# Optimization experiments

Hardware: AMD Instinct MI355X
Metric: run time of the kernel (lower is better)

The kernel has to match this reference:

```python
import jax, jax.numpy as jnp
import numpy as np
from jax.scipy.linalg import solve_triangular

REG = 1e-6  # reg_covar added to covariance diagonal
LOG2PI = float(np.log(2.0 * np.pi))
RESP_EPS = 10.0 * float(np.finfo(np.float32).eps)


def _log_gauss(X, means, covs):
    # X: [N,D], means: [K,D], covs: [K,D,D] -> per-sample per-component log N(x|mu_k, Sigma_k): [N,K]
    K, D = means.shape
    eye = jnp.eye(D, dtype=X.dtype)
    chol = jnp.linalg.cholesky(covs + REG * eye)                      # [K,D,D]
    diff = X[None, :, :] - means[:, None, :]                          # [K,N,D]
    sol = jax.vmap(lambda L, d: solve_triangular(L, d.T, lower=True))(chol, diff)  # [K,D,N]
    maha = jnp.sum(sol * sol, axis=1)                                 # [K,N]
    logdet = jnp.sum(jnp.log(jnp.diagonal(chol, axis1=1, axis2=2)), axis=1)  # [K] = 0.5*log|Sigma|
    return (-0.5 * (D * LOG2PI + maha) - logdet[:, None]).T           # [N,K]


def _em_step(X, weights, means, covs):
    N, D = X.shape
    # E-step: responsibilities via stable logsumexp
    lp = _log_gauss(X, means, covs) + jnp.log(weights)[None, :]       # [N,K]
    log_norm = jax.scipy.special.logsumexp(lp, axis=1)                # [N]
    resp = jnp.exp(lp - log_norm[:, None])                            # [N,K]
    # M-step (MLE)
    nk = resp.sum(axis=0) + RESP_EPS                                  # [K]
    new_w = nk / N
    new_means = (resp.T @ X) / nk[:, None]                            # [K,D]
    diff = X[None, :, :] - new_means[:, None, :]                      # [K,N,D]
    new_covs = jnp.einsum('kn,knd,kne->kde', resp.T, diff, diff) / nk[:, None, None]
    new_covs = new_covs + REG * jnp.eye(D, dtype=X.dtype)
    return new_w, new_means, new_covs


def reference(X, weights, means, covariances, n_iter):
    # Normalize provided weights (uniform init in the torch module)
    w0 = weights / jnp.sum(weights)

    def step(carry, _):
        w, m, c = carry
        return _em_step(X, w, m, c), None

    (w, m, c), _ = jax.lax.scan(step, (w0, means, covariances), xs=None, length=n_iter)
    # Final per-sample log-likelihood under the fitted mixture (lower bound)
    lp = _log_gauss(X, m, c) + jnp.log(w)[None, :]
    return jax.scipy.special.logsumexp(lp, axis=1)                    # [N]


def setup_inputs() -> dict:
    key = jax.random.key(0)
    kx, km = jax.random.split(key)
    N, D, K = 100000, 32, 16
    X = jax.random.normal(kx, (N, D), dtype=jnp.float32)
    weights = jnp.ones((K,), dtype=jnp.float32) / K
    means = jax.random.normal(km, (K, D), dtype=jnp.float32)
    covariances = jnp.tile(jnp.eye(D, dtype=jnp.float32)[None], (K, 1, 1))
    return {"X": X, "weights": weights, "means": means, "covariances": covariances, "n_iter": 5}
```

## Files before the change

kernel.cpp:

```cpp
#include <hip/hip_runtime.h>
#include <math.h>

#define REGC 1e-6f
#define LOG2PI 1.83787706640934534f
#define RESP_EPS 1.1920929e-6f

#define NPART_MAX 256
#define PART_K 1156
#define PART_BLK (16 * PART_K)
#define RS 16

typedef __attribute__((ext_vector_type(8))) short short8;
typedef __attribute__((ext_vector_type(4))) float f32x4;
typedef unsigned short ushort_t;
typedef unsigned int uint_t;

__device__ __forceinline__ ushort_t f2bf(float x) {
    uint_t u = __float_as_uint(x);
    uint_t r = (u + 0x7fffu + ((u >> 16) & 1u)) >> 16;
    return (ushort_t)r;
}
__device__ __forceinline__ float bf2f(ushort_t h) {
    return __uint_as_float(((uint_t)h) << 16);
}
__device__ __forceinline__ f32x4 shx4(f32x4 v, int m) {
    f32x4 r;
#pragma unroll
    for (int i = 0; i < 4; ++i) r[i] = __shfl_xor(v[i], m);
    return r;
}
__device__ __forceinline__ f32x4 sel4(bool s, f32x4 b, f32x4 a) {
    f32x4 r;
#pragma unroll
    for (int i = 0; i < 4; ++i) r[i] = s ? b[i] : a[i];
    return r;
}

__global__ void gmm_init(const float* __restrict__ w, const float* __restrict__ mu,
                         const float* __restrict__ cov, float* __restrict__ P0) {
    int t = blockIdx.x * 256 + threadIdx.x;
    if (t < 16) {
        float s = 0.f;
        for (int i = 0; i < 16; ++i) s += w[i];
        P0[t] = w[t] / s;
    } else if (t < 528) {
        P0[t] = mu[t - 16];
    } else if (t < 16912) {
        P0[t] = cov[t - 528];
    }
}

__global__ __launch_bounds__(256) void gmm_xsplit(const float* __restrict__ X,
                                                  ushort_t* __restrict__ Xh,
                                                  ushort_t* __restrict__ Xl,
                                                  ushort_t* __restrict__ XTH,
                                                  int N) {
    int chunk = blockIdx.x;
    int t = threadIdx.x;
    __shared__ float xsh[32][33];
    int s = t >> 3, q = t & 7;
    int n = chunk * 32 + s;
    float4 v = make_float4(0.f, 0.f, 0.f, 0.f);
    if (n < N) v = ((const float4*)(X + (size_t)n * 32))[q];
    float vv[4] = { v.x, v.y, v.z, v.w };
    xsh[s][q * 4 + 0] = v.x; xsh[s][q * 4 + 1] = v.y;
    xsh[s][q * 4 + 2] = v.z; xsh[s][q * 4 + 3] = v.w;
    if (n < N) {
        ushort_t h[4], l[4];
#pragma unroll
        for (int i = 0; i < 4; ++i) {
            h[i] = f2bf(vv[i]);
            l[i] = f2bf(vv[i] - bf2f(h[i]));
        }
        size_t o = (size_t)n * 32 + q * 4;
        uint2 hp = make_uint2((uint_t)h[0] | ((uint_t)h[1] << 16),
                              (uint_t)h[2] | ((uint_t)h[3] << 16));
        uint2 lp = make_uint2((uint_t)l[0] | ((uint_t)l[1] << 16),
                              (uint_t)l[2] | ((uint_t)l[3] << 16));
        *(uint2*)(Xh + o) = hp;
        *(uint2*)(Xl + o) = lp;
    }
    __syncthreads();
    int di = t >> 7;
    int lane = (t >> 1) & 63;
    int jj0 = (t & 1) * 4;
    int c = lane & 15, quad = lane >> 4;
    int d = di * 16 + c;
    ushort_t fh[4];
#pragma unroll
    for (int i = 0; i < 4; ++i) fh[i] = f2bf(xsh[quad * 8 + jj0 + i][d]);
    size_t fo = ((size_t)(chunk * 2 + di) * 64 + lane) * 8 + jj0;
    uint2 hp = make_uint2((uint_t)fh[0] | ((uint_t)fh[1] << 16),
                          (uint_t)fh[2] | ((uint_t)fh[3] << 16));
    *(uint2*)(XTH + fo) = hp;
}

__global__ __launch_bounds__(64) void gmm_prep(const float* __restrict__ P,
                                               ushort_t* __restrict__ Wh,
                                               ushort_t* __restrict__ Wl,
                                               float* __restrict__ Bv,
                                               float* __restrict__ Cc) {
    int k = blockIdx.x;
    int t = threadIdx.x;
    __shared__ float L[32][33];
    __shared__ float Ai[32][33];
    const float* cov = P + 528 + k * 1024;
    const float* mu  = P + 16 + k * 32;

#pragma unroll
    for (int rep = 0; rep < 16; ++rep) {
        int idx = rep * 64 + t;
        int i = idx >> 5, j = idx & 31;
        L[i][j] = cov[idx] + (i == j ? REGC : 0.f);
    }
    __syncthreads();

#pragma unroll
    for (int j = 0; j < 32; ++j) {
        float s = L[j][j];
#pragma unroll
        for (int p = 0; p < j; ++p) { float v = L[j][p]; s -= v * v; }
        float dj = sqrtf(s);
        if (t > j && t < 32) {
            float s2 = L[t][j];
#pragma unroll
            for (int p = 0; p < j; ++p) s2 -= L[t][p] * L[j][p];
            L[t][j] = s2 / dj;
        }
        if (t == j) L[j][j] = dj;
        __syncthreads();
    }

    if (t < 32) {
        float ai[32];
#pragma unroll
        for (int r = 0; r < 32; ++r) {
            float s = (r == t) ? 1.f : 0.f;
#pragma unroll
            for (int p = 0; p < r; ++p) s -= L[r][p] * ai[p];
            ai[r] = s / L[r][r];
        }
#pragma unroll
        for (int r = 0; r < 32; ++r) Ai[r][t] = ai[r];
    }
    __syncthreads();

#pragma unroll
    for (int rep = 0; rep < 16; ++rep) {
        int idx = rep * 64 + t;
        int i = idx >> 5, j = idx & 31;
        float v = Ai[i][j];
        ushort_t h = f2bf(v);
        Wh[(size_t)(k * 32 + i) * 32 + j] = h;
        Wl[(size_t)(k * 32 + i) * 32 + j] = f2bf(v - bf2f(h));
    }
    if (t < 32) {
        float s = 0.f;
#pragma unroll
        for (int j = 0; j < 32; ++j) s += Ai[t][j] * mu[j];
        Bv[k * 32 + t] = s;
    }
    float lv = (t < 32) ? logf(L[t & 31][t & 31]) : 0.f;
#pragma unroll
    for (int off = 1; off < 32; off <<= 1) lv += __shfl_xor(lv, off);
    if (t == 0) Cc[k] = logf(P[k]) - 0.5f * 32.0f * LOG2PI - lv;
}

__global__ __launch_bounds__(256, 2) void gmm_estep(const ushort_t* __restrict__ Xh,
                                                    const ushort_t* __restrict__ Xl,
                                                    const ushort_t* __restrict__ Wh,
                                                    const ushort_t* __restrict__ Wl,
                                                    const float* __restrict__ Bv,
                                                    const float* __restrict__ Cc,
                                                    float* __restrict__ resp,
                                                    float* __restrict__ out,
                                                    int N, int mode) {
    int t = threadIdx.x;
    int wave = t >> 6, lane = t & 63;
    int quad = lane >> 4, c = lane & 15;
    int wstart = (blockIdx.x * 4 + wave) * 32;
    if (wstart + 32 > N) wstart = (N >= 32) ? (N - 32) : 0;
    bool al4 = ((N & 3) == 0);

    size_t xo0 = (size_t)(wstart + c) * 32 + quad * 8;
    size_t xo1 = (size_t)(wstart + 16 + c) * 32 + quad * 8;
    short8 ah0 = *(const short8*)(Xh + xo0);
    short8 al0 = *(const short8*)(Xl + xo0);
    short8 ah1 = *(const short8*)(Xh + xo1);
    short8 al1 = *(const short8*)(Xl + xo1);

    f32x4 p0[2], p1[2], p2[2], p3[2], fin[2];

#pragma unroll
    for (int k = 0; k < 16; ++k) {
        size_t w0 = (size_t)(k * 32 + c) * 32 + quad * 8;
        size_t w1 = w0 + 512;
        short8 bh0 = *(const short8*)(Wh + w0);
        short8 bl0 = *(const short8*)(Wl + w0);
        short8 bh1 = *(const short8*)(Wh + w1);
        short8 bl1 = *(const short8*)(Wl + w1);
        float bv0 = Bv[k * 32 + c];
        float bv1 = Bv[k * 32 + 16 + c];
#pragma unroll
        for (int tt = 0; tt < 2; ++tt) {
            short8 ah = tt ? ah1 : ah0;
            short8 al = tt ? al1 : al0;
            f32x4 a0 = {0.f, 0.f, 0.f, 0.f};
            f32x4 a1 = {0.f, 0.f, 0.f, 0.f};
            a0 = __builtin_amdgcn_mfma_f32_16x16x32_bf16(ah, bh0, a0, 0, 0, 0);
            a0 = __builtin_amdgcn_mfma_f32_16x16x32_bf16(ah, bl0, a0, 0, 0, 0);
            a0 = __builtin_amdgcn_mfma_f32_16x16x32_bf16(al, bh0, a0, 0, 0, 0);
            a1 = __builtin_amdgcn_mfma_f32_16x16x32_bf16(ah, bh1, a1, 0, 0, 0);
            a1 = __builtin_amdgcn_mfma_f32_16x16x32_bf16(ah, bl1, a1, 0, 0, 0);
            a1 = __builtin_amdgcn_mfma_f32_16x16x32_bf16(al, bh1, a1, 0, 0, 0);
            f32x4 ms;
#pragma unroll
            for (int r = 0; r < 4; ++r) {
                float d0 = a0[r] - bv0;
                float d1 = a1[r] - bv1;
                ms[r] = fmaf(d0, d0, d1 * d1);
            }
            if ((k & 1) == 0) { p0[tt] = ms; }
            else {
                f32x4 a = p0[tt] + shx4(p0[tt], 1);
                f32x4 b = ms + shx4(ms, 1);
                f32x4 v = sel4((c & 1) != 0, b, a);
                if ((k & 2) == 0) { p1[tt] = v; }
                else {
                    a = p1[tt] + shx4(p1[tt], 2); b = v + shx4(v, 2); v = sel4((c & 2) != 0, b, a);
                    if ((k & 4) == 0) { p2[tt] = v; }
                    else {
                        a = p2[tt] + shx4(p2[tt], 4); b = v + shx4(v, 4); v = sel4((c & 4) != 0, b, a);
                        if ((k & 8) == 0) { p3[tt] = v; }
                        else {
                            a = p3[tt] + shx4(p3[tt], 8); b = v + shx4(v, 8);
                            fin[tt] = sel4((c & 8) != 0, b, a);
                        }
                    }
                }
            }
        }
    }

    float cc = Cc[c];
#pragma unroll
    for (int tt = 0; tt < 2; ++tt) {
        f32x4 lp;
#pragma unroll
        for (int r = 0; r < 4; ++r) lp[r] = cc - 0.5f * fin[tt][r];
        f32x4 mx = lp;
#pragma unroll
        for (int off = 1; off < 16; off <<= 1) {
            f32x4 s = shx4(mx, off);
#pragma unroll
            for (int r = 0; r < 4; ++r) mx[r] = fmaxf(mx[r], s[r]);
        }
        f32x4 e;
#pragma unroll
        for (int r = 0; r < 4; ++r) e[r] = __expf(lp[r] - mx[r]);
        f32x4 sm = e;
#pragma unroll
        for (int off = 1; off < 16; off <<= 1) sm = sm + shx4(sm, off);

        int nb = wstart + tt * 16 + quad * 4;
        if (mode) {
            if (c == 0) {
                f32x4 o;
#pragma unroll
                for (int r = 0; r < 4; ++r) o[r] = mx[r] + __logf(sm[r]);
                if (al4) *(f32x4*)(out + nb) = o;
                else { for (int r = 0; r < 4; ++r) out[nb + r] = o[r]; }
            }
        } else {
            f32x4 sv;
#pragma unroll
            for (int r = 0; r < 4; ++r) sv[r] = e[r] / sm[r];
            size_t off = (size_t)c * N + nb;
            if (al4) *(f32x4*)(resp + off) = sv;
            else { for (int r = 0; r < 4; ++r) resp[off + r] = sv[r]; }
        }
    }
}

__global__ __launch_bounds__(1024, 4) void gmm_moment(const ushort_t* __restrict__ XTH,
                                                      const float* __restrict__ resp,
                                                      float* __restrict__ part,
                                                      int N, int NC) {
    int t = threadIdx.x;
    int k = t >> 6;
    int lane = t & 63;
    int quad = lane >> 4, c = lane & 15;
    bool al4 = ((N & 3) == 0);

    f32x4 acc00 = {0.f,0.f,0.f,0.f}, acc01 = {0.f,0.f,0.f,0.f};
    f32x4 acc10 = {0.f,0.f,0.f,0.f}, acc11 = {0.f,0.f,0.f,0.f};
    float row0 = 0.f, row1 = 0.f, corner = 0.f;

#pragma unroll 1
    for (int chunk = blockIdx.x; chunk < NC; chunk += gridDim.x) {
        size_t fb = ((size_t)chunk * 2 * 64 + lane) * 8;
        short8 bh0 = *(const short8*)(XTH + fb);
        short8 bh1 = *(const short8*)(XTH + fb + 512);

        const float* rp = resp + (size_t)k * N + (size_t)chunk * 32 + quad * 8;
        float r[8];
        if (al4) {
            float4 ra = *(const float4*)rp;
            float4 rb = *(const float4*)(rp + 4);
            r[0]=ra.x; r[1]=ra.y; r[2]=ra.z; r[3]=ra.w;
            r[4]=rb.x; r[5]=rb.y; r[6]=rb.z; r[7]=rb.w;
        } else {
#pragma unroll
            for (int j = 0; j < 8; ++j) r[j] = rp[j];
        }
        corner += ((r[0]+r[1])+(r[2]+r[3])) + ((r[4]+r[5])+(r[6]+r[7]));

        short8 a0, a1;
#pragma unroll
        for (int jj = 0; jj < 8; ++jj) {
            float x0 = bf2f((ushort_t)bh0[jj]);
            float av0 = r[jj] * x0;
            a0[jj] = (short)f2bf(av0);
            row0 += av0;
            float x1 = bf2f((ushort_t)bh1[jj]);
            float av1 = r[jj] * x1;
            a1[jj] = (short)f2bf(av1);
            row1 += av1;
        }

        acc00 = __builtin_amdgcn_mfma_f32_16x16x32_bf16(a0, bh0, acc00, 0, 0, 0);
        acc01 = __builtin_amdgcn_mfma_f32_16x16x32_bf16(a0, bh1, acc01, 0, 0, 0);
        acc10 = __builtin_amdgcn_mfma_f32_16x16x32_bf16(a1, bh0, acc10, 0, 0, 0);
        acc11 = __builtin_amdgcn_mfma_f32_16x16x32_bf16(a1, bh1, acc11, 0, 0, 0);
    }

    row0 += __shfl_xor(row0, 16);  row0 += __shfl_xor(row0, 32);
    row1 += __shfl_xor(row1, 16);  row1 += __shfl_xor(row1, 32);
    corner += __shfl_xor(corner, 16);  corner += __shfl_xor(corner, 32);

    float* pb = part + ((size_t)blockIdx.x * 16 + k) * PART_K;
#pragma unroll
    for (int r = 0; r < 4; ++r) {
        pb[(quad * 4 + r) * 34 + c]            = acc00[r];
        pb[(quad * 4 + r) * 34 + 16 + c]       = acc01[r];
        pb[(16 + quad * 4 + r) * 34 + c]       = acc10[r];
        pb[(16 + quad * 4 + r) * 34 + 16 + c]  = acc11[r];
    }
    if (quad == 0) {
        pb[32 * 34 + c]      = row0;
        pb[32 * 34 + 16 + c] = row1;
    }
    if (lane == 0) pb[32 * 34 + 32] = corner;
}

__global__ __launch_bounds__(256) void gmm_reduce1(const float* __restrict__ part,
                                                   float* __restrict__ part2,
                                                   int npart) {
    int k = blockIdx.x, g = blockIdx.y;
    int nb = (npart + RS - 1) / RS;
    int b0 = g * nb;
    int b1 = b0 + nb; if (b1 > npart) b1 = npart;
    for (int idx = threadIdx.x; idx < PART_K; idx += 256) {
        float s = 0.f;
#pragma unroll 4
        for (int b = b0; b < b1; ++b)
            s += part[((size_t)b * 16 + k) * PART_K + idx];
        part2[((size_t)g * 16 + k) * PART_K + idx] = s;
    }
}

__global__ __launch_bounds__(256) void gmm_redfin_prep(const float* __restrict__ part2,
                                                       ushort_t* __restrict__ Wh,
                                                       ushort_t* __restrict__ Wl,
                                                       float* __restrict__ Bv,
                                                       float* __restrict__ Cc,
                                                       int N) {
    int k = blockIdx.x;
    int t = threadIdx.x;
    __shared__ float S[1156];
    __shared__ float L[32][33];
    __shared__ float Ai[32][33];

    for (int idx = t; idx < 1156; idx += 256) {
        float s = 0.f;
#pragma unroll
        for (int b = 0; b < RS; ++b)
            s += part2[((size_t)b * 16 + k) * PART_K + idx];
        S[idx] = s;
    }
    __syncthreads();
    float nk = S[32 * 34 + 32] + RESP_EPS;
    float inv = 1.f / nk;
    for (int idx = t; idx < 1024; idx += 256) {
        int i = idx >> 5, j = idx & 31;
        float mi = S[32 * 34 + i] * inv;
        float mj = S[32 * 34 + j] * inv;
        L[i][j] = S[i * 34 + j] * inv - mi * mj + ((i == j) ? 2.f * REGC : 0.f);
    }
    __syncthreads();

#pragma unroll
    for (int j = 0; j < 32; ++j) {
        if (t < 32) {
            float s = L[j][j];
#pragma unroll
            for (int p = 0; p < j; ++p) { float v = L[j][p]; s -= v * v; }
            float dj = sqrtf(s);
            if (t > j) {
                float s2 = L[t][j];
#pragma unroll
                for (int p = 0; p < j; ++p) s2 -= L[t][p] * L[j][p];
                L[t][j] = s2 / dj;
            }
            if (t == j) L[j][j] = dj;
        }
        __syncthreads();
    }

    if (t < 32) {
        float ai[32];
#pragma unroll
        for (int r = 0; r < 32; ++r) {
            float s = (r == t) ? 1.f : 0.f;
#pragma unroll
            for (int p = 0; p < r; ++p) s -= L[r][p] * ai[p];
            ai[r] = s / L[r][r];
        }
#pragma unroll
        for (int r = 0; r < 32; ++r) Ai[r][t] = ai[r];
    }
    __syncthreads();

#pragma unroll
    for (int rep = 0; rep < 4; ++rep) {
        int idx = rep * 256 + t;
        int i = idx >> 5, j = idx & 31;
        float v = Ai[i][j];
        ushort_t h = f2bf(v);
        Wh[(size_t)(k * 32 + i) * 32 + j] = h;
        Wl[(size_t)(k * 32 + i) * 32 + j] = f2bf(v - bf2f(h));
    }
    if (t < 32) {
        float s = 0.f;
#pragma unroll
        for (int j = 0; j < 32; ++j) s += Ai[t][j] * (S[32 * 34 + j] * inv);
        Bv[k * 32 + t] = s;
    }
    float lv = (t < 32) ? logf(L[t & 31][t & 31]) : 0.f;
#pragma unroll
    for (int off = 1; off < 32; off <<= 1) lv += __shfl_xor(lv, off);
    if (t == 0) Cc[k] = logf(nk / (float)N) - 0.5f * 32.0f * LOG2PI - lv;
}

extern "C" void kernel_launch(void* const* d_in, const int* in_sizes, int n_in,
                              void* d_out, int out_size, void* d_ws, size_t ws_size,
                              hipStream_t stream) {
    const float* X   = (const float*)d_in[0];
    const float* w   = (const float*)d_in[1];
    const float* mu  = (const float*)d_in[2];
    const float* cov = (const float*)d_in[3];
    const int NITER = 5;
    int N = in_sizes[0] / 32;
    int NC = (N + 31) / 32;

    float* ws = (float*)d_ws;
    float*    P0 = ws;
    float*    Bv = ws + 16912;
    float*    Cc = ws + 17424;
    ushort_t* Wh = (ushort_t*)(ws + 17440);
    ushort_t* Wl = (ushort_t*)(ws + 25632);
    ushort_t* Xh = (ushort_t*)(ws + 33824);
    ushort_t* Xl = (ushort_t*)(ws + 33824 + (size_t)16 * N);
    size_t xt0 = 33824 + (size_t)32 * N;
    size_t SZ  = (size_t)NC * 512;
    ushort_t* XTH = (ushort_t*)(ws + xt0);
    float*  resp = ws + xt0 + SZ;
    size_t p2base = xt0 + SZ + (size_t)16 * N;
    float*  part2 = ws + p2base;
    size_t pbase = p2base + (size_t)RS * 16 * PART_K;
    float*  part = ws + pbase;

    long long avail = (long long)(ws_size / 4) - (long long)pbase;
    int npart = (int)(avail / PART_BLK);
    if (npart > NPART_MAX) npart = NPART_MAX;
    if (npart < 1) npart = 1;

    float* out = (float*)d_out;

    int eblocks = ((N + 31) / 32 + 3) / 4;

    gmm_init<<<67, 256, 0, stream>>>(w, mu, cov, P0);
    gmm_xsplit<<<NC, 256, 0, stream>>>(X, Xh, Xl, XTH, N);
    gmm_prep<<<16, 64, 0, stream>>>(P0, Wh, Wl, Bv, Cc);

    for (int it = 0; it < NITER; ++it) {
        gmm_estep<<<eblocks, 256, 0, stream>>>(Xh, Xl, Wh, Wl, Bv, Cc, resp, out, N, 0);
        gmm_moment<<<npart, 1024, 0, stream>>>(XTH, resp, part, N, NC);
        dim3 r1(16, RS);
        gmm_reduce1<<<r1, 256, 0, stream>>>(part, part2, npart);
        gmm_redfin_prep<<<16, 256, 0, stream>>>(part2, Wh, Wl, Bv, Cc, N);
    }
    gmm_estep<<<eblocks, 256, 0, stream>>>(Xh, Xl, Wh, Wl, Bv, Cc, resp, out, N, 1);
}
```

Before: 478.1 us.

## Fuse whole EM loop into one cooperative persistent kernel with grid syncs

Replaces the chain of roughly twenty launches (init, split, prep, then per-iteration estep/moment/reduce/finalize) with a single cooperative kernel. It runs one 1024-thread block per 512 samples and uses grid.sync between phases. Responsibilities stay in shared memory instead of a global resp array, X fragments are loaded once into registers, and the moment partials feed directly into a 16-block Cholesky stage. This removes launch gaps and global resp traffic, but requires every block to be co-resident. The final reduction also reads about 196 partials serially per component in only 16 blocks, and the old multi-kernel path is kept as a fallback if the cooperative launch fails.

```diff
diff --git a/kernel.cpp b/kernel.cpp
--- a/kernel.cpp
+++ b/kernel.cpp
@@ -1,5 +1,8 @@
 #include <hip/hip_runtime.h>
+#include <hip/hip_cooperative_groups.h>
 #include <math.h>
+
+namespace cg = cooperative_groups;
 
 #define REGC 1e-6f
 #define LOG2PI 1.83787706640934534f
@@ -34,6 +37,325 @@
 #pragma unroll
     for (int i = 0; i < 4; ++i) r[i] = s ? b[i] : a[i];
     return r;
+}
+
+__device__ __forceinline__ void chol_emit(float* Ls, float* Aif, const float* mean,
+                                          float logwk, int k,
+                                          ushort_t* Wh, ushort_t* Wl,
+                                          float* Bv, float* Cc) {
+    int t = threadIdx.x;
+#pragma unroll
+    for (int j = 0; j < 32; ++j) {
+        if (t < 32) {
+            float s = Ls[j * 33 + j];
+#pragma unroll
+            for (int p = 0; p < j; ++p) { float v = Ls[j * 33 + p]; s -= v * v; }
+            float dj = sqrtf(s);
+            if (t > j) {
+                float s2 = Ls[t * 33 + j];
+#pragma unroll
+                for (int p = 0; p < j; ++p) s2 -= Ls[t * 33 + p] * Ls[j * 33 + p];
+                Ls[t * 33 + j] = s2 / dj;
+            }
+            if (t == j) Ls[j * 33 + j] = dj;
+        }
+        __syncthreads();
+    }
+    if (t < 32) {
+        float ai[32];
+#pragma unroll
+        for (int r = 0; r < 32; ++r) {
+            float s = (r == t) ? 1.f : 0.f;
+#pragma unroll
+            for (int p = 0; p < r; ++p) s -= Ls[r * 33 + p] * ai[p];
+            ai[r] = s / Ls[r * 33 + r];
+        }
+#pragma unroll
+        for (int r = 0; r < 32; ++r) Aif[r * 33 + t] = ai[r];
+    }
+    __syncthreads();
+    {
+        int i = t >> 5, j = t & 31;
+        float v = Aif[i * 33 + j];
+        ushort_t h = f2bf(v);
+        Wh[(size_t)(k * 32 + i) * 32 + j] = h;
+        Wl[(size_t)(k * 32 + i) * 32 + j] = f2bf(v - bf2f(h));
+    }
+    if (t < 32) {
+        float s = 0.f;
+#pragma unroll
+        for (int j = 0; j < 32; ++j) s += Aif[t * 33 + j] * mean[j];
+        Bv[k * 32 + t] = s;
+    }
+    float lv = (t < 32) ? logf(Ls[t * 33 + t]) : 0.f;
+#pragma unroll
+    for (int off = 1; off < 32; off <<= 1) lv += __shfl_xor(lv, off);
+    if (t == 0) Cc[k] = logwk - 0.5f * 32.0f * LOG2PI - lv;
+}
+
+__global__ __launch_bounds__(1024, 4) void gmm_mega(
+    const float* __restrict__ X, const float* __restrict__ w,
+    const float* __restrict__ mu, const float* __restrict__ cov,
+    ushort_t* __restrict__ Xh, ushort_t* __restrict__ Xl,
+    ushort_t* __restrict__ XTH,
+    ushort_t* __restrict__ Wh, ushort_t* __restrict__ Wl,
+    float* __restrict__ Bv, float* __restrict__ Cc,
+    float* __restrict__ part, float* __restrict__ out,
+    int N, int niter) {
+    cg::grid_group grid = cg::this_grid();
+    __shared__ float smem[16 * 516];
+    float (*rsh)[516] = (float (*)[516])smem;
+
+    int t = threadIdx.x;
+    int wave = t >> 6, lane = t & 63;
+    int quad = lane >> 4, c = lane & 15;
+    int bbase = (int)blockIdx.x * 512;
+    bool al4 = ((N & 3) == 0);
+
+#pragma unroll 1
+    for (int rr = 0; rr < 4; ++rr) {
+        int ch = rr * 4 + (t >> 8);
+        int tl = t & 255;
+        float* xsh = smem + (t >> 8) * 1056;
+        int gc = (int)blockIdx.x * 16 + ch;
+        int s = tl >> 3, q = tl & 7;
+        int n = gc * 32 + s;
+        float4 v = make_float4(0.f, 0.f, 0.f, 0.f);
+        if (n < N) v = ((const float4*)(X + (size_t)n * 32))[q];
+        xsh[s * 33 + q * 4 + 0] = v.x; xsh[s * 33 + q * 4 + 1] = v.y;
+        xsh[s * 33 + q * 4 + 2] = v.z; xsh[s * 33 + q * 4 + 3] = v.w;
+        if (n < N) {
+            float vv[4] = { v.x, v.y, v.z, v.w };
+            ushort_t h[4], l[4];
+#pragma unroll
+            for (int i = 0; i < 4; ++i) {
+                h[i] = f2bf(vv[i]);
+                l[i] = f2bf(vv[i] - bf2f(h[i]));
+            }
+            size_t o = (size_t)n * 32 + q * 4;
+            *(uint2*)(Xh + o) = make_uint2((uint_t)h[0] | ((uint_t)h[1] << 16),
+                                           (uint_t)h[2] | ((uint_t)h[3] << 16));
+            *(uint2*)(Xl + o) = make_uint2((uint_t)l[0] | ((uint_t)l[1] << 16),
+                                           (uint_t)l[2] | ((uint_t)l[3] << 16));
+        }
+        __syncthreads();
+        int di = tl >> 7;
+        int lane2 = (tl >> 1) & 63;
+        int jj0 = (tl & 1) * 4;
+        int c2 = lane2 & 15, quad2 = lane2 >> 4;
+        int d = di * 16 + c2;
+        ushort_t fh[4];
+#pragma unroll
+        for (int i2 = 0; i2 < 4; ++i2) fh[i2] = f2bf(xsh[(quad2 * 8 + jj0 + i2) * 33 + d]);
+        size_t fo = ((size_t)(gc * 2 + di) * 64 + lane2) * 8 + jj0;
+        *(uint2*)(XTH + fo) = make_uint2((uint_t)fh[0] | ((uint_t)fh[1] << 16),
+                                         (uint_t)fh[2] | ((uint_t)fh[3] << 16));
+        __syncthreads();
+    }
+
+    if (blockIdx.x < 16) {
+        int k = (int)blockIdx.x;
+        float* Ls = smem + 1156;
+        float* Aif = smem + 2212;
+        {
+            int i = t >> 5, j = t & 31;
+            Ls[i * 33 + j] = cov[(size_t)k * 1024 + t] + ((i == j) ? REGC : 0.f);
+        }
+        float wsum = 0.f;
+#pragma unroll
+        for (int i = 0; i < 16; ++i) wsum += w[i];
+        float logwk = logf(w[k] / wsum);
+        __syncthreads();
+        chol_emit(Ls, Aif, mu + (size_t)k * 32, logwk, k, Wh, Wl, Bv, Cc);
+    }
+    grid.sync();
+    __threadfence();
+
+    int wstart0 = bbase + wave * 32;
+    bool dup = (wstart0 + 32 > N);
+    int wst = dup ? ((N >= 32) ? N - 32 : 0) : wstart0;
+    size_t xo0 = (size_t)(wst + c) * 32 + quad * 8;
+    size_t xo1 = (size_t)(wst + 16 + c) * 32 + quad * 8;
+    short8 ah0 = *(const short8*)(Xh + xo0);
+    short8 al0 = *(const short8*)(Xl + xo0);
+    short8 ah1 = *(const short8*)(Xh + xo1);
+    short8 al1 = *(const short8*)(Xl + xo1);
+
+    for (int it = 0; it <= niter; ++it) {
+        bool last = (it == niter);
+        {
+            f32x4 p0[2], p1[2], p2[2], p3[2], fin[2];
+#pragma unroll
+            for (int k = 0; k < 16; ++k) {
+                size_t w0 = (size_t)(k * 32 + c) * 32 + quad * 8;
+                size_t w1 = w0 + 512;
+                short8 bh0 = *(const short8*)(Wh + w0);
+                short8 bl0 = *(const short8*)(Wl + w0);
+                short8 bh1 = *(const short8*)(Wh + w1);
+                short8 bl1 = *(const short8*)(Wl + w1);
+                float bv0 = Bv[k * 32 + c];
+                float bv1 = Bv[k * 32 + 16 + c];
+#pragma unroll
+                for (int tt = 0; tt < 2; ++tt) {
+                    short8 ah = tt ? ah1 : ah0;
+                    short8 al = tt ? al1 : al0;
+                    f32x4 a0 = {0.f, 0.f, 0.f, 0.f};
+                    f32x4 a1 = {0.f, 0.f, 0.f, 0.f};
+                    a0 = __builtin_amdgcn_mfma_f32_16x16x32_bf16(ah, bh0, a0, 0, 0, 0);
+                    a0 = __builtin_amdgcn_mfma_f32_16x16x32_bf16(ah, bl0, a0, 0, 0, 0);
+                    a0 = __builtin_amdgcn_mfma_f32_16x16x32_bf16(al, bh0, a0, 0, 0, 0);
+                    a1 = __builtin_amdgcn_mfma_f32_16x16x32_bf16(ah, bh1, a1, 0, 0, 0);
+                    a1 = __builtin_amdgcn_mfma_f32_16x16x32_bf16(ah, bl1, a1, 0, 0, 0);
+                    a1 = __builtin_amdgcn_mfma_f32_16x16x32_bf16(al, bh1, a1, 0, 0, 0);
+                    f32x4 ms;
+#pragma unroll
+                    for (int r = 0; r < 4; ++r) {
+                        float d0 = a0[r] - bv0;
+                        float d1 = a1[r] - bv1;
+                        ms[r] = fmaf(d0, d0, d1 * d1);
+                    }
+                    if ((k & 1) == 0) { p0[tt] = ms; }
+                    else {
+                        f32x4 a = p0[tt] + shx4(p0[tt], 1);
+                        f32x4 b = ms + shx4(ms, 1);
+                        f32x4 v = sel4((c & 1) != 0, b, a);
+                        if ((k & 2) == 0) { p1[tt] = v; }
+                        else {
+                            a = p1[tt] + shx4(p1[tt], 2); b = v + shx4(v, 2); v = sel4((c & 2) != 0, b, a);
+                            if ((k & 4) == 0) { p2[tt] = v; }
+                            else {
+                                a = p2[tt] + shx4(p2[tt], 4); b = v + shx4(v, 4); v = sel4((c & 4) != 0, b, a);
+                                if ((k & 8) == 0) { p3[tt] = v; }
+                                else {
+                                    a = p3[tt] + shx4(p3[tt], 8); b = v + shx4(v, 8);
+                                    fin[tt] = sel4((c & 8) != 0, b, a);
+                                }
+                            }
+                        }
+                    }
+                }
+            }
+            float ccv = Cc[c];
+#pragma unroll
+            for (int tt = 0; tt < 2; ++tt) {
+                f32x4 lp;
+#pragma unroll
+                for (int r = 0; r < 4; ++r) lp[r] = ccv - 0.5f * fin[tt][r];
+                f32x4 mx = lp;
+#pragma unroll
+                for (int off = 1; off < 16; off <<= 1) {
+                    f32x4 s = shx4(mx, off);
+#pragma unroll
+                    for (int r = 0; r < 4; ++r) mx[r] = fmaxf(mx[r], s[r]);
+                }
+                f32x4 e;
+#pragma unroll
+                for (int r = 0; r < 4; ++r) e[r] = __expf(lp[r] - mx[r]);
+                f32x4 sm = e;
+#pragma unroll
+                for (int off = 1; off < 16; off <<= 1) sm = sm + shx4(sm, off);
+
+                if (last) {
+                    if (c == 0) {
+                        int nb = wst + tt * 16 + quad * 4;
+                        f32x4 o;
+#pragma unroll
+                        for (int r = 0; r < 4; ++r) o[r] = mx[r] + __logf(sm[r]);
+                        if (al4) *(f32x4*)(out + nb) = o;
+                        else { for (int r = 0; r < 4; ++r) out[nb + r] = o[r]; }
+                    }
+                } else {
+                    int pos = wave * 32 + tt * 16 + quad * 4;
+#pragma unroll
+                    for (int r = 0; r < 4; ++r)
+                        rsh[c][pos + r] = dup ? 0.f : e[r] / sm[r];
+                }
+            }
+        }
+        if (last) break;
+        __syncthreads();
+
+        {
+            f32x4 m00 = {0.f,0.f,0.f,0.f}, m01 = {0.f,0.f,0.f,0.f};
+            f32x4 m10 = {0.f,0.f,0.f,0.f}, m11 = {0.f,0.f,0.f,0.f};
+            float row0 = 0.f, row1 = 0.f, corner = 0.f;
+#pragma unroll 4
+            for (int ch = 0; ch < 16; ++ch) {
+                size_t fb = (((size_t)((int)blockIdx.x * 16 + ch)) * 128 + lane) * 8;
+                short8 bh0 = *(const short8*)(XTH + fb);
+                short8 bh1 = *(const short8*)(XTH + fb + 512);
+                float r8[8];
+#pragma unroll
+                for (int jj = 0; jj < 8; ++jj) r8[jj] = rsh[wave][ch * 32 + quad * 8 + jj];
+                corner += ((r8[0]+r8[1])+(r8[2]+r8[3])) + ((r8[4]+r8[5])+(r8[6]+r8[7]));
+                short8 a0, a1;
+#pragma unroll
+                for (int jj = 0; jj < 8; ++jj) {
+                    float x0 = bf2f((ushort_t)bh0[jj]);
+                    float av0 = r8[jj] * x0;
+                    a0[jj] = (short)f2bf(av0);
+                    row0 += av0;
+                    float x1 = bf2f((ushort_t)bh1[jj]);
+                    float av1 = r8[jj] * x1;
+                    a1[jj] = (short)f2bf(av1);
+                    row1 += av1;
+                }
+                m00 = __builtin_amdgcn_mfma_f32_16x16x32_bf16(a0, bh0, m00, 0, 0, 0);
+                m01 = __builtin_amdgcn_mfma_f32_16x16x32_bf16(a0, bh1, m01, 0, 0, 0);
+                m10 = __builtin_amdgcn_mfma_f32_16x16x32_bf16(a1, bh0, m10, 0, 0, 0);
+                m11 = __builtin_amdgcn_mfma_f32_16x16x32_bf16(a1, bh1, m11, 0, 0, 0);
+            }
+            row0 += __shfl_xor(row0, 16);  row0 += __shfl_xor(row0, 32);
+            row1 += __shfl_xor(row1, 16);  row1 += __shfl_xor(row1, 32);
+            corner += __shfl_xor(corner, 16);  corner += __shfl_xor(corner, 32);
+
+            float* pb = part + ((size_t)blockIdx.x * 16 + wave) * PART_K;
+#pragma unroll
+            for (int r = 0; r < 4; ++r) {
+                pb[(quad * 4 + r) * 34 + c]           = m00[r];
+                pb[(quad * 4 + r) * 34 + 16 + c]      = m01[r];
+                pb[(16 + quad * 4 + r) * 34 + c]      = m10[r];
+                pb[(16 + quad * 4 + r) * 34 + 16 + c] = m11[r];
+            }
+            if (quad == 0) {
+                pb[32 * 34 + c]      = row0;
+                pb[32 * 34 + 16 + c] = row1;
+            }
+            if (lane == 0) pb[32 * 34 + 32] = corner;
+        }
+        grid.sync();
+        __threadfence();
+
+        if (blockIdx.x < 16) {
+            int k = (int)blockIdx.x;
+            float* S_ = smem;
+            float* Ls = smem + 1156;
+            float* Aif = smem + 2212;
+            float* mean = smem + 3268;
+            int nblk = (int)gridDim.x;
+            for (int idx = t; idx < 1121; idx += 1024) {
+                float s = 0.f;
+#pragma unroll 4
+                for (int b = 0; b < nblk; ++b)
+                    s += part[((size_t)b * 16 + k) * PART_K + idx];
+                S_[idx] = s;
+            }
+            __syncthreads();
+            float nk = S_[32 * 34 + 32] + RESP_EPS;
+            float inv = 1.f / nk;
+            {
+                int i = t >> 5, j = t & 31;
+                float mi = S_[32 * 34 + i] * inv;
+                float mj = S_[32 * 34 + j] * inv;
+                Ls[i * 33 + j] = S_[i * 34 + j] * inv - mi * mj + ((i == j) ? 2.f * REGC : 0.f);
+            }
+            if (t < 32) mean[t] = S_[32 * 34 + t] * inv;
+            __syncthreads();
+            chol_emit(Ls, Aif, mean, logf(nk / (float)N), k, Wh, Wl, Bv, Cc);
+        }
+        grid.sync();
+        __threadfence();
+    }
 }
 
 __global__ void gmm_init(const float* __restrict__ w, const float* __restrict__ mu,
@@ -73,12 +395,10 @@
             l[i] = f2bf(vv[i] - bf2f(h[i]));
         }
         size_t o = (size_t)n * 32 + q * 4;
-        uint2 hp = make_uint2((uint_t)h[0] | ((uint_t)h[1] << 16),
-                              (uint_t)h[2] | ((uint_t)h[3] << 16));
-        uint2 lp = make_uint2((uint_t)l[0] | ((uint_t)l[1] << 16),
-                              (uint_t)l[2] | ((uint_t)l[3] << 16));
-        *(uint2*)(Xh + o) = hp;
-        *(uint2*)(Xl + o) = lp;
+        *(uint2*)(Xh + o) = make_uint2((uint_t)h[0] | ((uint_t)h[1] << 16),
+                                       (uint_t)h[2] | ((uint_t)h[3] << 16));
+        *(uint2*)(Xl + o) = make_uint2((uint_t)l[0] | ((uint_t)l[1] << 16),
+                                       (uint_t)l[2] | ((uint_t)l[3] << 16));
     }
     __syncthreads();
     int di = t >> 7;
@@ -90,9 +410,8 @@
 #pragma unroll
     for (int i = 0; i < 4; ++i) fh[i] = f2bf(xsh[quad * 8 + jj0 + i][d]);
     size_t fo = ((size_t)(chunk * 2 + di) * 64 + lane) * 8 + jj0;
-    uint2 hp = make_uint2((uint_t)fh[0] | ((uint_t)fh[1] << 16),
-                          (uint_t)fh[2] | ((uint_t)fh[3] << 16));
-    *(uint2*)(XTH + fo) = hp;
+    *(uint2*)(XTH + fo) = make_uint2((uint_t)fh[0] | ((uint_t)fh[1] << 16),
+                                     (uint_t)fh[2] | ((uint_t)fh[3] << 16));
 }
 
 __global__ __launch_bounds__(64) void gmm_prep(const float* __restrict__ P,
@@ -104,17 +423,15 @@
     int t = threadIdx.x;
     __shared__ float L[32][33];
     __shared__ float Ai[32][33];
-    const float* cov = P + 528 + k * 1024;
-    const float* mu  = P + 16 + k * 32;
-
+    const float* cv = P + 528 + k * 1024;
+    const float* muk = P + 16 + k * 32;
 #pragma unroll
     for (int rep = 0; rep < 16; ++rep) {
         int idx = rep * 64 + t;
         int i = idx >> 5, j = idx & 31;
-        L[i][j] = cov[idx] + (i == j ? REGC : 0.f);
+        L[i][j] = cv[idx] + (i == j ? REGC : 0.f);
     }
     __syncthreads();
-
 #pragma unroll
     for (int j = 0; j < 32; ++j) {
         float s = L[j][j];
@@ -130,7 +447,6 @@
         if (t == j) L[j][j] = dj;
         __syncthreads();
     }
-
     if (t < 32) {
         float ai[32];
 #pragma unroll
@@ -144,7 +460,6 @@
         for (int r = 0; r < 32; ++r) Ai[r][t] = ai[r];
     }
     __syncthreads();
-
 #pragma unroll
     for (int rep = 0; rep < 16; ++rep) {
         int idx = rep * 64 + t;
@@ -157,7 +472,7 @@
     if (t < 32) {
         float s = 0.f;
 #pragma unroll
-        for (int j = 0; j < 32; ++j) s += Ai[t][j] * mu[j];
+        for (int j = 0; j < 32; ++j) s += Ai[t][j] * muk[j];
         Bv[k * 32 + t] = s;
     }
     float lv = (t < 32) ? logf(L[t & 31][t & 31]) : 0.f;
@@ -190,7 +505,6 @@
     short8 al1 = *(const short8*)(Xl + xo1);
 
     f32x4 p0[2], p1[2], p2[2], p3[2], fin[2];
-
 #pragma unroll
     for (int k = 0; k < 16; ++k) {
         size_t w0 = (size_t)(k * 32 + c) * 32 + quad * 8;
@@ -241,13 +555,12 @@
             }
         }
     }
-
-    float cc = Cc[c];
+    float ccv = Cc[c];
 #pragma unroll
     for (int tt = 0; tt < 2; ++tt) {
         f32x4 lp;
 #pragma unroll
-        for (int r = 0; r < 4; ++r) lp[r] = cc - 0.5f * fin[tt][r];
+        for (int r = 0; r < 4; ++r) lp[r] = ccv - 0.5f * fin[tt][r];
         f32x4 mx = lp;
 #pragma unroll
         for (int off = 1; off < 16; off <<= 1) {
@@ -261,7 +574,6 @@
         f32x4 sm = e;
 #pragma unroll
         for (int off = 1; off < 16; off <<= 1) sm = sm + shx4(sm, off);
-
         int nb = wstart + tt * 16 + quad * 4;
         if (mode) {
             if (c == 0) {
@@ -291,17 +603,14 @@
     int lane = t & 63;
     int quad = lane >> 4, c = lane & 15;
     bool al4 = ((N & 3) == 0);
-
     f32x4 acc00 = {0.f,0.f,0.f,0.f}, acc01 = {0.f,0.f,0.f,0.f};
     f32x4 acc10 = {0.f,0.f,0.f,0.f}, acc11 = {0.f,0.f,0.f,0.f};
     float row0 = 0.f, row1 = 0.f, corner = 0.f;
-
 #pragma unroll 1
     for (int chunk = blockIdx.x; chunk < NC; chunk += gridDim.x) {
         size_t fb = ((size_t)chunk * 2 * 64 + lane) * 8;
         short8 bh0 = *(const short8*)(XTH + fb);
         short8 bh1 = *(const short8*)(XTH + fb + 512);
-
         const float* rp = resp + (size_t)k * N + (size_t)chunk * 32 + quad * 8;
         float r[8];
         if (al4) {
@@ -314,7 +623,6 @@
             for (int j = 0; j < 8; ++j) r[j] = rp[j];
         }
         corner += ((r[0]+r[1])+(r[2]+r[3])) + ((r[4]+r[5])+(r[6]+r[7]));
-
         short8 a0, a1;
 #pragma unroll
         for (int jj = 0; jj < 8; ++jj) {
@@ -327,24 +635,21 @@
             a1[jj] = (short)f2bf(av1);
             row1 += av1;
         }
-
         acc00 = __builtin_amdgcn_mfma_f32_16x16x32_bf16(a0, bh0, acc00, 0, 0, 0);
         acc01 = __builtin_amdgcn_mfma_f32_16x16x32_bf16(a0, bh1, acc01, 0, 0, 0);
         acc10 = __builtin_amdgcn_mfma_f32_16x16x32_bf16(a1, bh0, acc10, 0, 0, 0);
         acc11 = __builtin_amdgcn_mfma_f32_16x16x32_bf16(a1, bh1, acc11, 0, 0, 0);
     }
-
     row0 += __shfl_xor(row0, 16);  row0 += __shfl_xor(row0, 32);
     row1 += __shfl_xor(row1, 16);  row1 += __shfl_xor(row1, 32);
     corner += __shfl_xor(corner, 16);  corner += __shfl_xor(corner, 32);
-
     float* pb = part + ((size_t)blockIdx.x * 16 + k) * PART_K;
 #pragma unroll
     for (int r = 0; r < 4; ++r) {
-        pb[(quad * 4 + r) * 34 + c]            = acc00[r];
-        pb[(quad * 4 + r) * 34 + 16 + c]       = acc01[r];
-        pb[(16 + quad * 4 + r) * 34 + c]       = acc10[r];
-        pb[(16 + quad * 4 + r) * 34 + 16 + c]  = acc11[r];
+        pb[(quad * 4 + r) * 34 + c]           = acc00[r];
+        pb[(quad * 4 + r) * 34 + 16 + c]      = acc01[r];
+        pb[(16 + quad * 4 + r) * 34 + c]      = acc10[r];
+        pb[(16 + quad * 4 + r) * 34 + 16 + c] = acc11[r];
     }
     if (quad == 0) {
         pb[32 * 34 + c]      = row0;
@@ -380,7 +685,6 @@
     __shared__ float S[1156];
     __shared__ float L[32][33];
     __shared__ float Ai[32][33];
-
     for (int idx = t; idx < 1156; idx += 256) {
         float s = 0.f;
 #pragma unroll
@@ -398,7 +702,6 @@
         L[i][j] = S[i * 34 + j] * inv - mi * mj + ((i == j) ? 2.f * REGC : 0.f);
     }
     __syncthreads();
-
 #pragma unroll
     for (int j = 0; j < 32; ++j) {
         if (t < 32) {
@@ -416,7 +719,6 @@
         }
         __syncthreads();
     }
-
     if (t < 32) {
         float ai[32];
 #pragma unroll
@@ -430,7 +732,6 @@
         for (int r = 0; r < 32; ++r) Ai[r][t] = ai[r];
     }
     __syncthreads();
-
 #pragma unroll
     for (int rep = 0; rep < 4; ++rep) {
         int idx = rep * 256 + t;
@@ -459,21 +760,23 @@
     const float* w   = (const float*)d_in[1];
     const float* mu  = (const float*)d_in[2];
     const float* cov = (const float*)d_in[3];
-    const int NITER = 5;
+    int niter = 5;
     int N = in_sizes[0] / 32;
     int NC = (N + 31) / 32;
+    int MB = (N + 511) / 512;
+    if (MB < 16) MB = 16;
 
     float* ws = (float*)d_ws;
     float*    P0 = ws;
-    float*    Bv = ws + 16912;
-    float*    Cc = ws + 17424;
-    ushort_t* Wh = (ushort_t*)(ws + 17440);
-    ushort_t* Wl = (ushort_t*)(ws + 25632);
-    ushort_t* Xh = (ushort_t*)(ws + 33824);
-    ushort_t* Xl = (ushort_t*)(ws + 33824 + (size_t)16 * N);
+    float*    Bvp = ws + 16912;
+    float*    Ccp = ws + 17424;
+    ushort_t* Whp = (ushort_t*)(ws + 17440);
+    ushort_t* Wlp = (ushort_t*)(ws + 25632);
+    ushort_t* Xhp = (ushort_t*)(ws + 33824);
+    ushort_t* Xlp = (ushort_t*)(ws + 33824 + (size_t)16 * N);
     size_t xt0 = 33824 + (size_t)32 * N;
-    size_t SZ  = (size_t)NC * 512;
-    ushort_t* XTH = (ushort_t*)(ws + xt0);
+    size_t SZ  = (size_t)MB * 16 * 512;
+    ushort_t* XTHp = (ushort_t*)(ws + xt0);
     float*  resp = ws + xt0 + SZ;
     size_t p2base = xt0 + SZ + (size_t)16 * N;
     float*  part2 = ws + p2base;
@@ -487,18 +790,27 @@
 
     float* out = (float*)d_out;
 
-    int eblocks = ((N + 31) / 32 + 3) / 4;
-
-    gmm_init<<<67, 256, 0, stream>>>(w, mu, cov, P0);
-    gmm_xsplit<<<NC, 256, 0, stream>>>(X, Xh, Xl, XTH, N);
-    gmm_prep<<<16, 64, 0, stream>>>(P0, Wh, Wl, Bv, Cc);
-
-    for (int it = 0; it < NITER; ++it) {
-        gmm_estep<<<eblocks, 256, 0, stream>>>(Xh, Xl, Wh, Wl, Bv, Cc, resp, out, N, 0);
-        gmm_moment<<<npart, 1024, 0, stream>>>(XTH, resp, part, N, NC);
-        dim3 r1(16, RS);
-        gmm_reduce1<<<r1, 256, 0, stream>>>(part, part2, npart);
-        gmm_redfin_prep<<<16, 256, 0, stream>>>(part2, Wh, Wl, Bv, Cc, N);
-    }
-    gmm_estep<<<eblocks, 256, 0, stream>>>(Xh, Xl, Wh, Wl, Bv, Cc, resp, out, N, 1);
-}
+    hipError_t cerr = hipErrorUnknown;
+    if (MB <= 256 && npart >= MB && (N & 31) == 0) {
+        void* kargs[] = { (void*)&X, (void*)&w, (void*)&mu, (void*)&cov,
+                          (void*)&Xhp, (void*)&Xlp, (void*)&XTHp,
+                          (void*)&Whp, (void*)&Wlp, (void*)&Bvp, (void*)&Ccp,
+                          (void*)&part, (void*)&out, (void*)&N, (void*)&niter };
+        cerr = hipLaunchCooperativeKernel((const void*)gmm_mega, dim3(MB), dim3(1024),
+                                          kargs, 0, stream);
+    }
+    if (cerr != hipSuccess) {
+        int eblocks = ((N + 31) / 32 + 3) / 4;
+        gmm_init<<<67, 256, 0, stream>>>(w, mu, cov, P0);
+        gmm_xsplit<<<NC, 256, 0, stream>>>(X, Xhp, Xlp, XTHp, N);
+        gmm_prep<<<16, 64, 0, stream>>>(P0, Whp, Wlp, Bvp, Ccp);
+        for (int it = 0; it < niter; ++it) {
+            gmm_estep<<<eblocks, 256, 0, stream>>>(Xhp, Xlp, Whp, Wlp, Bvp, Ccp, resp, out, N, 0);
+            gmm_moment<<<npart, 1024, 0, stream>>>(XTHp, resp, part, N, NC);
+            dim3 r1(16, RS);
+            gmm_reduce1<<<r1, 256, 0, stream>>>(part, part2, npart);
+            gmm_redfin_prep<<<16, 256, 0, stream>>>(part2, Whp, Wlp, Bvp, Ccp, N);
+        }
+        gmm_estep<<<eblocks, 256, 0, stream>>>(Xhp, Xlp, Whp, Wlp, Bvp, Ccp, resp, out, N, 1);
+    }
+}
```

After: 1.809 ms. 3.78x slower.
